# Kernel optimization log

Measured on AMD Instinct MI355X. Metric: run time of the kernel, lower is better.

## Reference

```python
import jax, jax.numpy as jnp
import numpy as np

DT = 0.2   # dt
T = 30     # free-phase relaxation steps


def rho(x):
    return jnp.clip(x, 0.0, 1.0)


def rhop(x):
    return ((x >= 0.0) & (x <= 1.0)).astype(x.dtype)


def setup_inputs() -> dict:
    key = jax.random.key(0)
    ks = jax.random.split(key, 10)
    B = 2048
    L = [1024, 2048, 2048, 2048]  # fcLayers
    s0 = jax.random.uniform(ks[0], (B, L[0]), dtype=jnp.float32)
    s1 = jax.random.uniform(ks[1], (B, L[1]), dtype=jnp.float32)
    s2 = jax.random.uniform(ks[2], (B, L[2]), dtype=jnp.float32)
    data = jax.random.uniform(ks[3], (B, L[3]), dtype=jnp.float32)
    # W[i] = Linear(fcLayers[i+1], fcLayers[i]) -> weight [L[i], L[i+1]], fan_in = L[i+1]
    W0 = jax.random.normal(ks[4], (L[0], L[1]), dtype=jnp.float32) / np.float32(np.sqrt(L[1]))
    b0 = jax.random.normal(ks[5], (L[0],), dtype=jnp.float32) * np.float32(0.01)
    W1 = jax.random.normal(ks[6], (L[1], L[2]), dtype=jnp.float32) / np.float32(np.sqrt(L[2]))
    b1 = jax.random.normal(ks[7], (L[1],), dtype=jnp.float32) * np.float32(0.01)
    W2 = jax.random.normal(ks[8], (L[2], L[3]), dtype=jnp.float32) / np.float32(np.sqrt(L[3]))
    b2 = jax.random.normal(ks[9], (L[2],), dtype=jnp.float32) * np.float32(0.01)
    return {"s0": s0, "s1": s1, "s2": s2, "data": data,
            "W0": W0, "b0": b0, "W1": W1, "b1": b1, "W2": W2, "b2": b2}


def reference(s0, s1, s2, data, W0, b0, W1, b1, W2, b2):
    # Free-phase (beta=None, target=None, loss='MSE') -> stepper_c iterated T times.
    # s = [s0, s1, s2, data]; data (last element) is never updated.
    rd = rho(data)  # fixed input drive, precomputed once

    def step(carry, _):
        s0, s1, s2 = carry
        r0, r1, r2 = rho(s0), rho(s1), rho(s2)
        # dsdt[0] = -s0 + rhop(s0) * W0(rho(s1))
        d0 = -s0 + rhop(s0) * (r1 @ W0.T + b0)
        # dsdt[1] = -s1 + rhop(s1) * ( W1(rho(s2)) + rho(s0) @ W0 )
        d1 = -s1 + rhop(s1) * (r2 @ W1.T + b1 + r0 @ W0)
        # dsdt[2] = -s2 + rhop(s2) * ( W2(rho(data)) + rho(s1) @ W1 )
        d2 = -s2 + rhop(s2) * (rd @ W2.T + b2 + r1 @ W1)
        n0 = jnp.clip(s0 + DT * d0, 0.0, 1.0)
        n1 = jnp.clip(s1 + DT * d1, 0.0, 1.0)
        n2 = jnp.clip(s2 + DT * d2, 0.0, 1.0)
        return (n0, n1, n2), None

    (f0, f1, f2), _ = jax.lax.scan(step, (s0, s1, s2), None, length=T)
    return (f0, f1, f2)
```

## Files before the change

kernel.cpp:

```cpp
#include <hip/hip_runtime.h>
#include <stdint.h>

#define BM 128
#define BN 128
#define BK 64

typedef __bf16 bf16x8 __attribute__((ext_vector_type(8)));
typedef float f32x4 __attribute__((ext_vector_type(4)));

__device__ __forceinline__ float bf2f(uint16_t u) {
  union { uint32_t u32; float f; } x; x.u32 = ((uint32_t)u) << 16; return x.f;
}
__device__ __forceinline__ uint16_t f2bf(float f) {
  uint32_t x = __float_as_uint(f);
  uint32_t r = (x + 0x7FFFu + ((x >> 16) & 1u)) >> 16;
  return (uint16_t)r;
}

__device__ __forceinline__ void gload_lds16(const uint16_t* g, uint16_t* l) {
  __builtin_amdgcn_global_load_lds(
      (const __attribute__((address_space(1))) uint32_t*)g,
      (__attribute__((address_space(3))) uint32_t*)l, 16, 0, 0);
}

__device__ __forceinline__ void gemm_tile(
    const uint16_t* __restrict__ A, int ldA,
    const uint16_t* __restrict__ Bt, int ldB,
    int m0, int n0, int K,
    uint16_t* ldsA, uint16_t* ldsB, f32x4 acc[4][4])
{
  const int t  = threadIdx.x;
  const int ln = t & 63;
  const int wv = t >> 6;
  const int wr = wv >> 1, wc = wv & 1;

  const int row = t >> 3;
  const int gc  = (t & 7) ^ (row & 7);
  const uint16_t* ga = A  + (size_t)(m0 + row) * ldA + (gc << 3);
  const uint16_t* gb = Bt + (size_t)(n0 + row) * ldB + (gc << 3);
  uint16_t* la = ldsA + (t << 3);
  uint16_t* lb = ldsB + (t << 3);

  for (int kt = 0; kt < K; kt += BK) {
    __syncthreads();
#pragma unroll
    for (int c = 0; c < 4; ++c) {
      gload_lds16(ga + (size_t)(c * 32) * ldA, la + c * 2048);
      gload_lds16(gb + (size_t)(c * 32) * ldB, lb + c * 2048);
    }
    ga += BK; gb += BK;
    __syncthreads();

#pragma unroll
    for (int kk = 0; kk < 2; ++kk) {
      const int kc = (kk << 2) + (ln >> 4);
      const int sw = (kc ^ (ln & 7)) << 3;
      bf16x8 af[4], bfr[4];
#pragma unroll
      for (int mt = 0; mt < 4; ++mt)
        af[mt] = *(const bf16x8*)&ldsA[((wr << 6) + (mt << 4) + (ln & 15)) * BK + sw];
#pragma unroll
      for (int nt = 0; nt < 4; ++nt)
        bfr[nt] = *(const bf16x8*)&ldsB[((wc << 6) + (nt << 4) + (ln & 15)) * BK + sw];
#pragma unroll
      for (int mt = 0; mt < 4; ++mt)
#pragma unroll
        for (int nt = 0; nt < 4; ++nt)
          acc[mt][nt] = __builtin_amdgcn_mfma_f32_16x16x32_bf16(
              af[mt], bfr[nt], acc[mt][nt], 0, 0, 0);
    }
  }
}

__global__ void step_kernel(
    const uint16_t* __restrict__ s0b_c, const uint16_t* __restrict__ s1b_c,
    const uint16_t* __restrict__ s2b_c,
    uint16_t* __restrict__ s0b_n, uint16_t* __restrict__ s1b_n,
    uint16_t* __restrict__ s2b_n,
    const uint16_t* __restrict__ W0b, const uint16_t* __restrict__ W0Tb,
    const uint16_t* __restrict__ W1b, const uint16_t* __restrict__ W1Tb,
    const float* __restrict__ b0, const float* __restrict__ b1,
    const float* __restrict__ c2f,
    float* __restrict__ s0f, float* __restrict__ s1f, float* __restrict__ s2f)
{
  __shared__ uint16_t ldsA[BM * BK];
  __shared__ uint16_t ldsB[BN * BK];

  f32x4 acc[4][4];
  const f32x4 z = {0.f, 0.f, 0.f, 0.f};
#pragma unroll
  for (int i = 0; i < 4; ++i)
#pragma unroll
    for (int j = 0; j < 4; ++j) acc[i][j] = z;

  const int x = blockIdx.x & 7;
  const int j = blockIdx.x >> 3;
  const int g = x & 3;
  const int h = x >> 2;
  int mode, bm, bn;
  if (j < 16) {
    mode = 0; bm = (g << 2) + (j >> 2); bn = (h << 2) + (j & 3);
    gemm_tile(s1b_c, 2048, W0b, 2048, bm * BM, bn * BN, 2048, ldsA, ldsB, acc);
  } else if (j < 48) {
    mode = 1; const int u = j - 16; bm = (g << 2) + (u >> 3); bn = (h << 3) + (u & 7);
    gemm_tile(s2b_c, 2048, W1b, 2048, bm * BM, bn * BN, 2048, ldsA, ldsB, acc);
    gemm_tile(s0b_c, 1024, W0Tb, 1024, bm * BM, bn * BN, 1024, ldsA, ldsB, acc);
  } else {
    mode = 2; const int u = j - 48; bm = (g << 2) + (u >> 3); bn = (h << 3) + (u & 7);
    gemm_tile(s1b_c, 2048, W1Tb, 2048, bm * BM, bn * BN, 2048, ldsA, ldsB, acc);
  }

  const int t = threadIdx.x, wv = t >> 6, ln = t & 63;
  const int wr = wv >> 1, wc = wv & 1;
  const int rb = (ln >> 4) << 2, cc = ln & 15;
  const int m0 = bm * BM, n0 = bn * BN;

#pragma unroll
  for (int mt = 0; mt < 4; ++mt) {
#pragma unroll
    for (int nt = 0; nt < 4; ++nt) {
      const int gn = n0 + (wc << 6) + (nt << 4) + cc;
      float add = 0.f;
      if (mode == 0) add = b0[gn];
      else if (mode == 1) add = b1[gn];
#pragma unroll
      for (int r = 0; r < 4; ++r) {
        const int gm = m0 + (wr << 6) + (mt << 4) + rb + r;
        const float pre = acc[mt][nt][r];
        if (mode == 0) {
          const size_t ix = (size_t)gm * 1024 + gn;
          float nv = 0.8f * s0f[ix] + 0.2f * (pre + add);
          nv = fminf(fmaxf(nv, 0.f), 1.f);
          s0f[ix] = nv;
          s0b_n[ix] = f2bf(nv);
        } else if (mode == 1) {
          const size_t ix = (size_t)gm * 2048 + gn;
          float nv = 0.8f * s1f[ix] + 0.2f * (pre + add);
          nv = fminf(fmaxf(nv, 0.f), 1.f);
          s1f[ix] = nv;
          s1b_n[ix] = f2bf(nv);
        } else {
          const size_t ix = (size_t)gm * 2048 + gn;
          float nv = 0.8f * s2f[ix] + 0.2f * (pre + c2f[ix]);
          nv = fminf(fmaxf(nv, 0.f), 1.f);
          s2f[ix] = nv;
          s2b_n[ix] = f2bf(nv);
        }
      }
    }
  }
}

__global__ void c2_kernel(const uint16_t* __restrict__ datab,
                          const uint16_t* __restrict__ W2b,
                          const float* __restrict__ b2,
                          float* __restrict__ c2f)
{
  __shared__ uint16_t ldsA[BM * BK];
  __shared__ uint16_t ldsB[BN * BK];
  f32x4 acc[4][4];
  const f32x4 z = {0.f, 0.f, 0.f, 0.f};
#pragma unroll
  for (int i = 0; i < 4; ++i)
#pragma unroll
    for (int j = 0; j < 4; ++j) acc[i][j] = z;

  const int bm = blockIdx.x >> 4, bn = blockIdx.x & 15;
  gemm_tile(datab, 2048, W2b, 2048, bm * BM, bn * BN, 2048, ldsA, ldsB, acc);

  const int t = threadIdx.x, wv = t >> 6, ln = t & 63;
  const int wr = wv >> 1, wc = wv & 1;
  const int rb = (ln >> 4) << 2, cc = ln & 15;
  const int m0 = bm * BM, n0 = bn * BN;
#pragma unroll
  for (int mt = 0; mt < 4; ++mt)
#pragma unroll
    for (int nt = 0; nt < 4; ++nt) {
      const int gn = n0 + (wc << 6) + (nt << 4) + cc;
      const float bb = b2[gn];
#pragma unroll
      for (int r = 0; r < 4; ++r) {
        const int gm = m0 + (wr << 6) + (mt << 4) + rb + r;
        c2f[(size_t)gm * 2048 + gn] = acc[mt][nt][r] + bb;
      }
    }
}

__global__ void conv_k(const float* __restrict__ src, uint16_t* __restrict__ dst)
{
  const size_t i4 = ((size_t)blockIdx.x * 256 + threadIdx.x) << 2;
  const float4 v = *(const float4*)(src + i4);
  ushort4 o;
  o.x = f2bf(v.x); o.y = f2bf(v.y); o.z = f2bf(v.z); o.w = f2bf(v.w);
  *(ushort4*)(dst + i4) = o;
}

__global__ void convT_k(const float* __restrict__ src, uint16_t* __restrict__ dst,
                        int ldS, int ldD)
{
  __shared__ uint16_t tile[32][33];
  const int r0 = blockIdx.y * 32, c0 = blockIdx.x * 32;
  tile[threadIdx.y][threadIdx.x] =
      f2bf(src[(size_t)(r0 + threadIdx.y) * ldS + c0 + threadIdx.x]);
  __syncthreads();
  dst[(size_t)(c0 + threadIdx.y) * ldD + r0 + threadIdx.x] = tile[threadIdx.x][threadIdx.y];
}

__global__ void init_state(const float* __restrict__ in,
                           float* __restrict__ sf, uint16_t* __restrict__ sb)
{
  const size_t i4 = ((size_t)blockIdx.x * 256 + threadIdx.x) << 2;
  const float4 v = *(const float4*)(in + i4);
  *(float4*)(sf + i4) = v;
  ushort4 o;
  o.x = f2bf(v.x); o.y = f2bf(v.y); o.z = f2bf(v.z); o.w = f2bf(v.w);
  *(ushort4*)(sb + i4) = o;
}

extern "C" void kernel_launch(void* const* d_in, const int* in_sizes, int n_in,
                              void* d_out, int out_size, void* d_ws, size_t ws_size,
                              hipStream_t stream) {
  const float* s0   = (const float*)d_in[0];
  const float* s1   = (const float*)d_in[1];
  const float* s2   = (const float*)d_in[2];
  const float* data = (const float*)d_in[3];
  const float* W0   = (const float*)d_in[4];
  const float* b0   = (const float*)d_in[5];
  const float* W1   = (const float*)d_in[6];
  const float* b1   = (const float*)d_in[7];
  const float* W2   = (const float*)d_in[8];
  const float* b2   = (const float*)d_in[9];

  float* s0f = (float*)d_out;
  float* s1f = s0f + 2048ull * 1024;
  float* s2f = s1f + 2048ull * 2048;

  char* ws = (char*)d_ws;
  size_t off = 0;
  auto alloc = [&](size_t bytes) -> char* {
    char* p = ws + off; off += (bytes + 255) & ~(size_t)255; return p;
  };
  uint16_t* W0b    = (uint16_t*)alloc(1024ull * 2048 * 2);
  uint16_t* W0Tb   = (uint16_t*)alloc(2048ull * 1024 * 2);
  uint16_t* W1b    = (uint16_t*)alloc(2048ull * 2048 * 2);
  uint16_t* W1Tb   = (uint16_t*)alloc(2048ull * 2048 * 2);
  float*    c2f    = (float*)   alloc(2048ull * 2048 * 4);
  uint16_t* s0b[2] = { (uint16_t*)alloc(2048ull * 1024 * 2),
                       (uint16_t*)alloc(2048ull * 1024 * 2) };
  uint16_t* s1b[2] = { (uint16_t*)alloc(2048ull * 2048 * 2),
                       (uint16_t*)alloc(2048ull * 2048 * 2) };
  uint16_t* s2b[2] = { (uint16_t*)alloc(2048ull * 2048 * 2),
                       (uint16_t*)alloc(2048ull * 2048 * 2) };
  (void)ws_size; (void)in_sizes; (void)n_in; (void)out_size;

  conv_k<<<1024 * 2048 / 1024, 256, 0, stream>>>(W0, W0b);
  conv_k<<<2048 * 2048 / 1024, 256, 0, stream>>>(W1, W1b);
  dim3 tb(32, 32);
  convT_k<<<dim3(64, 32), tb, 0, stream>>>(W0, W0Tb, 2048, 1024);
  convT_k<<<dim3(64, 64), tb, 0, stream>>>(W1, W1Tb, 2048, 2048);
  conv_k<<<2048 * 2048 / 1024, 256, 0, stream>>>(data, s1b[1]);
  conv_k<<<2048 * 2048 / 1024, 256, 0, stream>>>(W2, s2b[1]);
  c2_kernel<<<256, 256, 0, stream>>>(s1b[1], s2b[1], b2, c2f);

  init_state<<<2048 * 1024 / 1024, 256, 0, stream>>>(s0, s0f, s0b[0]);
  init_state<<<2048 * 2048 / 1024, 256, 0, stream>>>(s1, s1f, s1b[0]);
  init_state<<<2048 * 2048 / 1024, 256, 0, stream>>>(s2, s2f, s2b[0]);

  for (int it = 0; it < 30; ++it) {
    const int c = it & 1, n = c ^ 1;
    step_kernel<<<640, 256, 0, stream>>>(
        s0b[c], s1b[c], s2b[c], s0b[n], s1b[n], s2b[n],
        W0b, W0Tb, W1b, W1Tb, b0, b1, c2f, s0f, s1f, s2f);
  }
}
```

Baseline: 2.413 ms.

## Double-buffer LDS tiles in GEMM mainloop with explicit vmcnt waits

Turns the single-buffered global-to-LDS GEMM loop into a two-stage ping-pong pipeline. The next K tile is loaded asynchronously while the current one is consumed, using partial vmcnt waits and raw barriers in place of two full __syncthreads per tile. It also raises wave priority around the MFMA block and adds launch bounds of 2 blocks per CU. The aim is to hide global load latency behind matrix math. The cost is doubling per-block LDS to 64KB, which can limit occupancy.

Result: slower. 3.675 ms (+52.3%).

```diff
diff --git a/kernel.cpp b/kernel.cpp
--- a/kernel.cpp
+++ b/kernel.cpp
@@ -4,6 +4,7 @@
 #define BM 128
 #define BN 128
 #define BK 64
+#define NTHREADS 256
 
 typedef __bf16 bf16x8 __attribute__((ext_vector_type(8)));
 typedef float f32x4 __attribute__((ext_vector_type(4)));
@@ -23,11 +24,24 @@
       (__attribute__((address_space(3))) uint32_t*)l, 16, 0, 0);
 }
 
+__device__ __forceinline__ void waitv8() {
+  asm volatile("s_waitcnt vmcnt(8)" ::: "memory");
+  __builtin_amdgcn_sched_barrier(0);
+}
+__device__ __forceinline__ void waitv0() {
+  asm volatile("s_waitcnt vmcnt(0)" ::: "memory");
+  __builtin_amdgcn_sched_barrier(0);
+}
+__device__ __forceinline__ void sbar() {
+  __builtin_amdgcn_s_barrier();
+  __builtin_amdgcn_sched_barrier(0);
+}
+
 __device__ __forceinline__ void gemm_tile(
     const uint16_t* __restrict__ A, int ldA,
     const uint16_t* __restrict__ Bt, int ldB,
     int m0, int n0, int K,
-    uint16_t* ldsA, uint16_t* ldsB, f32x4 acc[4][4])
+    uint16_t* lds0, uint16_t* lds1, f32x4 acc[4][4])
 {
   const int t  = threadIdx.x;
   const int ln = t & 63;
@@ -36,21 +50,26 @@
 
   const int row = t >> 3;
   const int gc  = (t & 7) ^ (row & 7);
-  const uint16_t* ga = A  + (size_t)(m0 + row) * ldA + (gc << 3);
-  const uint16_t* gb = Bt + (size_t)(n0 + row) * ldB + (gc << 3);
-  uint16_t* la = ldsA + (t << 3);
-  uint16_t* lb = ldsB + (t << 3);
-
-  for (int kt = 0; kt < K; kt += BK) {
-    __syncthreads();
+  const uint16_t* gA = A  + (size_t)(m0 + row) * ldA + (gc << 3);
+  const uint16_t* gB = Bt + (size_t)(n0 + row) * ldB + (gc << 3);
+
+  uint16_t* const bufs[2] = { lds0, lds1 };
+
+  auto STAGE = [&](int tile, uint16_t* buf) {
+    const uint16_t* ga = gA + tile * BK;
+    const uint16_t* gb = gB + tile * BK;
+    uint16_t* la = buf + (t << 3);
+    uint16_t* lb = buf + BM * BK + (t << 3);
 #pragma unroll
     for (int c = 0; c < 4; ++c) {
       gload_lds16(ga + (size_t)(c * 32) * ldA, la + c * 2048);
       gload_lds16(gb + (size_t)(c * 32) * ldB, lb + c * 2048);
     }
-    ga += BK; gb += BK;
-    __syncthreads();
-
+  };
+
+  auto COMPUTE = [&](const uint16_t* buf) {
+    const uint16_t* bA = buf;
+    const uint16_t* bB = buf + BM * BK;
 #pragma unroll
     for (int kk = 0; kk < 2; ++kk) {
       const int kc = (kk << 2) + (ln >> 4);
@@ -58,21 +77,41 @@
       bf16x8 af[4], bfr[4];
 #pragma unroll
       for (int mt = 0; mt < 4; ++mt)
-        af[mt] = *(const bf16x8*)&ldsA[((wr << 6) + (mt << 4) + (ln & 15)) * BK + sw];
+        af[mt] = *(const bf16x8*)&bA[((wr << 6) + (mt << 4) + (ln & 15)) * BK + sw];
 #pragma unroll
       for (int nt = 0; nt < 4; ++nt)
-        bfr[nt] = *(const bf16x8*)&ldsB[((wc << 6) + (nt << 4) + (ln & 15)) * BK + sw];
+        bfr[nt] = *(const bf16x8*)&bB[((wc << 6) + (nt << 4) + (ln & 15)) * BK + sw];
+      __builtin_amdgcn_s_setprio(1);
 #pragma unroll
       for (int mt = 0; mt < 4; ++mt)
 #pragma unroll
         for (int nt = 0; nt < 4; ++nt)
           acc[mt][nt] = __builtin_amdgcn_mfma_f32_16x16x32_bf16(
               af[mt], bfr[nt], acc[mt][nt], 0, 0, 0);
+      __builtin_amdgcn_s_setprio(0);
     }
+  };
+
+  const int nt = K >> 6;
+
+  STAGE(0, bufs[0]);
+  STAGE(1, bufs[1]);
+  waitv8(); sbar();
+
+  for (int i = 0; i < nt - 2; ++i) {
+    COMPUTE(bufs[i & 1]);
+    sbar();
+    STAGE(i + 2, bufs[i & 1]);
+    waitv8(); sbar();
   }
-}
-
-__global__ void step_kernel(
+  COMPUTE(bufs[nt & 1]);
+  sbar();
+  waitv0(); sbar();
+  COMPUTE(bufs[(nt - 1) & 1]);
+  sbar();
+}
+
+__global__ void __launch_bounds__(NTHREADS, 2) step_kernel(
     const uint16_t* __restrict__ s0b_c, const uint16_t* __restrict__ s1b_c,
     const uint16_t* __restrict__ s2b_c,
     uint16_t* __restrict__ s0b_n, uint16_t* __restrict__ s1b_n,
@@ -83,8 +122,7 @@
     const float* __restrict__ c2f,
     float* __restrict__ s0f, float* __restrict__ s1f, float* __restrict__ s2f)
 {
-  __shared__ uint16_t ldsA[BM * BK];
-  __shared__ uint16_t ldsB[BN * BK];
+  __shared__ uint16_t lds[2][(BM + BN) * BK];
 
   f32x4 acc[4][4];
   const f32x4 z = {0.f, 0.f, 0.f, 0.f};
@@ -100,14 +138,14 @@
   int mode, bm, bn;
   if (j < 16) {
     mode = 0; bm = (g << 2) + (j >> 2); bn = (h << 2) + (j & 3);
-    gemm_tile(s1b_c, 2048, W0b, 2048, bm * BM, bn * BN, 2048, ldsA, ldsB, acc);
+    gemm_tile(s1b_c, 2048, W0b, 2048, bm * BM, bn * BN, 2048, lds[0], lds[1], acc);
   } else if (j < 48) {
     mode = 1; const int u = j - 16; bm = (g << 2) + (u >> 3); bn = (h << 3) + (u & 7);
-    gemm_tile(s2b_c, 2048, W1b, 2048, bm * BM, bn * BN, 2048, ldsA, ldsB, acc);
-    gemm_tile(s0b_c, 1024, W0Tb, 1024, bm * BM, bn * BN, 1024, ldsA, ldsB, acc);
+    gemm_tile(s2b_c, 2048, W1b, 2048, bm * BM, bn * BN, 2048, lds[0], lds[1], acc);
+    gemm_tile(s0b_c, 1024, W0Tb, 1024, bm * BM, bn * BN, 1024, lds[0], lds[1], acc);
   } else {
     mode = 2; const int u = j - 48; bm = (g << 2) + (u >> 3); bn = (h << 3) + (u & 7);
-    gemm_tile(s1b_c, 2048, W1Tb, 2048, bm * BM, bn * BN, 2048, ldsA, ldsB, acc);
+    gemm_tile(s1b_c, 2048, W1Tb, 2048, bm * BM, bn * BN, 2048, lds[0], lds[1], acc);
   }
 
   const int t = threadIdx.x, wv = t >> 6, ln = t & 63;
@@ -151,13 +189,13 @@
   }
 }
 
-__global__ void c2_kernel(const uint16_t* __restrict__ datab,
-                          const uint16_t* __restrict__ W2b,
-                          const float* __restrict__ b2,
-                          float* __restrict__ c2f)
-{
-  __shared__ uint16_t ldsA[BM * BK];
-  __shared__ uint16_t ldsB[BN * BK];
+__global__ void __launch_bounds__(NTHREADS, 2) c2_kernel(
+    const uint16_t* __restrict__ datab,
+    const uint16_t* __restrict__ W2b,
+    const float* __restrict__ b2,
+    float* __restrict__ c2f)
+{
+  __shared__ uint16_t lds[2][(BM + BN) * BK];
   f32x4 acc[4][4];
   const f32x4 z = {0.f, 0.f, 0.f, 0.f};
 #pragma unroll
@@ -166,7 +204,7 @@
     for (int j = 0; j < 4; ++j) acc[i][j] = z;
 
   const int bm = blockIdx.x >> 4, bn = blockIdx.x & 15;
-  gemm_tile(datab, 2048, W2b, 2048, bm * BM, bn * BN, 2048, ldsA, ldsB, acc);
+  gemm_tile(datab, 2048, W2b, 2048, bm * BM, bn * BN, 2048, lds[0], lds[1], acc);
 
   const int t = threadIdx.x, wv = t >> 6, ln = t & 63;
   const int wr = wv >> 1, wc = wv & 1;
@@ -260,7 +298,7 @@
   convT_k<<<dim3(64, 64), tb, 0, stream>>>(W1, W1Tb, 2048, 2048);
   conv_k<<<2048 * 2048 / 1024, 256, 0, stream>>>(data, s1b[1]);
   conv_k<<<2048 * 2048 / 1024, 256, 0, stream>>>(W2, s2b[1]);
-  c2_kernel<<<256, 256, 0, stream>>>(s1b[1], s2b[1], b2, c2f);
+  c2_kernel<<<256, NTHREADS, 0, stream>>>(s1b[1], s2b[1], b2, c2f);
 
   init_state<<<2048 * 1024 / 1024, 256, 0, stream>>>(s0, s0f, s0b[0]);
   init_state<<<2048 * 2048 / 1024, 256, 0, stream>>>(s1, s1f, s1b[0]);
@@ -268,7 +306,7 @@
 
   for (int it = 0; it < 30; ++it) {
     const int c = it & 1, n = c ^ 1;
-    step_kernel<<<640, 256, 0, stream>>>(
+    step_kernel<<<640, NTHREADS, 0, stream>>>(
         s0b[c], s1b[c], s2b[c], s0b[n], s1b[n], s2b[n],
         W0b, W0Tb, W1b, W1Tb, b0, b1, c2f, s0f, s1f, s2f);
   }
```
